# Optimization experiments

Measured on AMD Instinct MI355X. Metric: run time of the kernel, lower is better.

The kernel has to match this reference:

```python
import jax, jax.numpy as jnp
import numpy as np

B, T, D = 1, 2048, 4096
H, G = 32, 8
HD = D // H          # 128
REP = H // G         # 4
KV_DIM = 2 * HD * G  # 2048


def setup_inputs() -> dict:
    key = jax.random.key(0)
    k0, k1, k2, k3 = jax.random.split(key, 4)
    x = jax.random.normal(k0, (B, T, D), dtype=jnp.float32)
    Wq = jax.random.normal(k1, (D, D), dtype=jnp.float32) * 0.02
    Wkv = jax.random.normal(k2, (D, KV_DIM), dtype=jnp.float32) * 0.02
    Wo = jax.random.normal(k3, (D, D), dtype=jnp.float32) * 0.02
    bo = jnp.zeros((D,), dtype=jnp.float32)
    return {"x": x, "Wq": Wq, "Wkv": Wkv, "Wo": Wo, "bo": bo}


def reference(x, Wq, Wkv, Wo, bo):
    b, t, d = x.shape
    # projections (qkv_bias=False)
    q = jnp.dot(x, Wq).reshape(b, t, H, HD).transpose(0, 2, 1, 3)        # (b,H,t,hd)
    kv = jnp.dot(x, Wkv).reshape(b, t, G, 2, HD).transpose(2, 3, 0, 1, 4)  # (G,2,b,t,hd)
    k, v = kv[:, 0], kv[:, 1]                                             # (G,b,t,hd)
    # faithful to torch: unsqueeze+repeat then flat view(b, H, t, hd)
    k = jnp.broadcast_to(k[:, :, None], (G, b, REP, t, HD)).reshape(b, H, t, HD)
    v = jnp.broadcast_to(v[:, :, None], (G, b, REP, t, HD)).reshape(b, H, t, HD)
    # attention: mask then scale, matching original order
    scores = jnp.einsum('bhqd,bhkd->bhqk', q, k)                          # (b,H,t,t)
    causal = jnp.triu(jnp.ones((t, t), dtype=bool), 1)
    scores = jnp.where(causal[None, None], -jnp.inf, scores)
    weights = jax.nn.softmax(scores * (1.0 / HD ** 0.5), axis=-1)
    ctx = jnp.einsum('bhqk,bhkd->bhqd', weights, v)                       # (b,H,t,hd)
    ctx = ctx.transpose(0, 2, 1, 3).reshape(b, t, d)
    return jnp.dot(ctx, Wo) + bo
```

## Files before the change

kernel.cpp:

```cpp
#include <hip/hip_runtime.h>

#define T_SEQ 2048
#define D_MODEL 4096
#define NH 32
#define NG 8
#define HD 128

typedef unsigned short u16;
typedef __bf16 bf16x8 __attribute__((ext_vector_type(8)));
typedef float f32x4 __attribute__((ext_vector_type(4)));

#define AS1 __attribute__((address_space(1)))
#define AS3 __attribute__((address_space(3)))

__device__ __forceinline__ void async_cp16(const u16* g, u16* l) {
  __builtin_amdgcn_global_load_lds((AS1 void*)g, (AS3 void*)l, 16, 0, 0);
}

__device__ __forceinline__ u16 f2bf(float f){
  union { float f; unsigned x; } v; v.f = f;
  unsigned r = v.x + 0x7FFFu + ((v.x >> 16) & 1u);
  return (u16)(r >> 16);
}
__device__ __forceinline__ u16 to_bf(float f){ return f2bf(f); }
__device__ __forceinline__ u16 to_bf(u16 u){ return u; }

__global__ __launch_bounds__(256) void cvt_k(const float* __restrict__ in,
                                             u16* __restrict__ out, int n4)
{
  int i = blockIdx.x * 256 + threadIdx.x;
  if (i >= n4) return;
  float4 v = *(const float4*)&in[(size_t)i * 4];
  short4 o;
  o.x = (short)f2bf(v.x); o.y = (short)f2bf(v.y);
  o.z = (short)f2bf(v.z); o.w = (short)f2bf(v.w);
  *(short4*)&out[(size_t)i * 4] = o;
}

template<typename TIN>
__global__ __launch_bounds__(256) void transpose_k(const TIN* __restrict__ in,
                                                   u16* __restrict__ out, int R, int C)
{
  int z = blockIdx.z;
  in  += (size_t)z * R * C;
  out += (size_t)z * R * C;
  __shared__ __align__(16) u16 tile[32][36];
  int c0 = blockIdx.x * 32, r0 = blockIdx.y * 32;
  int t = threadIdx.x;
  int lr = t >> 3, lc = (t & 7) * 4;
  const TIN* src = &in[(size_t)(r0 + lr) * C + c0 + lc];
  #pragma unroll
  for (int i = 0; i < 4; i++) tile[lr][lc + i] = to_bf(src[i]);
  __syncthreads();
  short4 v;
  v.x = (short)tile[lc + 0][lr];
  v.y = (short)tile[lc + 1][lr];
  v.z = (short)tile[lc + 2][lr];
  v.w = (short)tile[lc + 3][lr];
  *(short4*)&out[(size_t)(c0 + lr) * R + r0 + lc] = v;
}

template<int MODE>
__global__ __launch_bounds__(256) void gemm_k(
    const u16* __restrict__ A, const u16* __restrict__ BT,
    u16* __restrict__ Cout, u16* __restrict__ Kout, u16* __restrict__ Vout,
    float* __restrict__ Fout, const float* __restrict__ bias, int K, int N)
{
  __shared__ __align__(16) u16 sA[2 * 128 * 64];
  __shared__ __align__(16) u16 sB[2 * 128 * 64];
  const int t = threadIdx.x;
  const int lane = t & 63, wave = t >> 6;
  const int quad = lane >> 4, lm = lane & 15;
  const int wm = wave >> 1, wn = wave & 1;
  const int m0 = blockIdx.y * 128, n0 = blockIdx.x * 128;
  const int ntk = K >> 6;
  const f32x4 fzero = {0.f, 0.f, 0.f, 0.f};

  const int sr_sub = lane >> 3;
  const int sgl = (lane & 7) ^ sr_sub;

  f32x4 acc[4][4];
  #pragma unroll
  for (int i = 0; i < 4; i++)
    #pragma unroll
    for (int j = 0; j < 4; j++) acc[i][j] = fzero;

  auto stage = [&](int td) {
    const int k0 = td << 6;
    u16* dA = sA + (td & 1) * (128 * 64);
    u16* dB = sB + (td & 1) * (128 * 64);
    #pragma unroll
    for (int c = 0; c < 4; c++) {
      int r = c * 32 + wave * 8 + sr_sub;
      async_cp16(&A [(size_t)(m0 + r) * K + k0 + sgl * 8], &dA[(c * 256 + wave * 64) * 8]);
      async_cp16(&BT[(size_t)(n0 + r) * K + k0 + sgl * 8], &dB[(c * 256 + wave * 64) * 8]);
    }
  };

  stage(0);
  stage(1);

  for (int ti = 0; ti < ntk; ++ti) {
    if (ti + 1 < ntk) { asm volatile("s_waitcnt vmcnt(8)" ::: "memory"); }
    else             { asm volatile("s_waitcnt vmcnt(0)" ::: "memory"); }
    __builtin_amdgcn_s_barrier();
    asm volatile("" ::: "memory");

    const u16* cA = sA + (ti & 1) * (128 * 64);
    const u16* cB = sB + (ti & 1) * (128 * 64);

    __builtin_amdgcn_s_setprio(1);
    #pragma unroll
    for (int kb = 0; kb < 2; kb++) {
      bf16x8 af[4], bfr[4];
      #pragma unroll
      for (int mt = 0; mt < 4; mt++) {
        int row = wm * 64 + mt * 16 + lm;
        af[mt] = *(const bf16x8*)&cA[row * 64 + (((kb * 4 + quad) ^ (lm & 7)) * 8)];
      }
      #pragma unroll
      for (int nt = 0; nt < 4; nt++) {
        int row = wn * 64 + nt * 16 + lm;
        bfr[nt] = *(const bf16x8*)&cB[row * 64 + (((kb * 4 + quad) ^ (lm & 7)) * 8)];
      }
      #pragma unroll
      for (int mt = 0; mt < 4; mt++)
        #pragma unroll
        for (int nt = 0; nt < 4; nt++)
          acc[mt][nt] = __builtin_amdgcn_mfma_f32_16x16x32_bf16(af[mt], bfr[nt], acc[mt][nt], 0, 0, 0);
    }
    __builtin_amdgcn_s_setprio(0);

    __builtin_amdgcn_s_barrier();
    asm volatile("" ::: "memory");
    if (ti + 2 < ntk) stage(ti + 2);
  }

  #pragma unroll
  for (int mt = 0; mt < 4; mt++) {
    #pragma unroll
    for (int nt = 0; nt < 4; nt++) {
      int gcol = n0 + wn * 64 + nt * 16 + lm;
      int grow0 = m0 + wm * 64 + mt * 16 + quad * 4;
      if (MODE == 1 && ((gcol >> 7) & 1)) {
        int g = gcol >> 8, hd = gcol & 127;
        short4 pv;
        pv.x = (short)f2bf(acc[mt][nt][0]);
        pv.y = (short)f2bf(acc[mt][nt][1]);
        pv.z = (short)f2bf(acc[mt][nt][2]);
        pv.w = (short)f2bf(acc[mt][nt][3]);
        *(short4*)&Vout[((size_t)g * HD + hd) * T_SEQ + grow0] = pv;
      } else {
        #pragma unroll
        for (int r = 0; r < 4; r++) {
          int grow = grow0 + r;
          float v = acc[mt][nt][r];
          if (MODE == 0) {
            Cout[(size_t)grow * N + gcol] = f2bf(v);
          } else if (MODE == 1) {
            int g = gcol >> 8, hd = gcol & 127;
            Kout[((size_t)g * T_SEQ + grow) * HD + hd] = f2bf(v);
          } else {
            Fout[(size_t)grow * N + gcol] = v + bias[gcol];
          }
        }
      }
    }
  }
}

__global__ __launch_bounds__(256) void attn_k(
    const u16* __restrict__ Q, const u16* __restrict__ Kb,
    const u16* __restrict__ Vt, u16* __restrict__ ctx)
{
  __shared__ __align__(16) u16 sK[2 * 64 * 128];
  __shared__ __align__(16) u16 sV[2 * 128 * 64];
  __shared__ __align__(16) u16 sP[4 * 16 * 72];
  const int t = threadIdx.x;
  const int lane = t & 63, wave = t >> 6;
  const int quad = lane >> 4, lm = lane & 15;

  const int id = blockIdx.x + gridDim.x * blockIdx.y;
  const int g = id & 7;
  const int idx = id >> 3;
  const int h = g * 4 + (idx & 3);
  const int q0 = (31 - (idx >> 2)) * 64;
  const int nt = (q0 >> 6) + 1;

  const float scale = 0.088388347648318447f;
  const float C1 = scale * 1.4426950408889634f;
  const float C2 = -14.0f * 1.4426950408889634f;
  const f32x4 fzero = {0.f, 0.f, 0.f, 0.f};

  bf16x8 aq[4];
  {
    const u16* qp = Q + (size_t)(q0 + wave * 16 + lm) * D_MODEL + h * HD + quad * 8;
    #pragma unroll
    for (int kb = 0; kb < 4; kb++) aq[kb] = *(const bf16x8*)(qp + kb * 32);
  }
  f32x4 o[8];
  #pragma unroll
  for (int i = 0; i < 8; i++) o[i] = fzero;
  float l4[4];
  #pragma unroll
  for (int r = 0; r < 4; r++) l4[r] = 0.f;

  const u16* Kg = Kb + (size_t)g * T_SEQ * HD;
  const u16* Vg = Vt + (size_t)g * HD * T_SEQ;
  u16* sPw = sP + wave * 16 * 72;

  const int k_r_sub = lane >> 4;
  const int v_r_sub = lane >> 3;
  const int v_gl = (lane & 7) ^ v_r_sub;

  auto stage = [&](int td) {
    const int kv0 = td << 6;
    u16* dK = sK + (td & 1) * (64 * 128);
    u16* dV = sV + (td & 1) * (128 * 64);
    #pragma unroll
    for (int c = 0; c < 4; c++) {
      int rk = c * 16 + wave * 4 + k_r_sub;
      int kgl = (lane & 15) ^ (rk & 7);
      async_cp16(&Kg[(size_t)(kv0 + rk) * HD + kgl * 8], &dK[(c * 256 + wave * 64) * 8]);
      int rv = c * 32 + wave * 8 + v_r_sub;
      async_cp16(&Vg[(size_t)rv * T_SEQ + kv0 + v_gl * 8], &dV[(c * 256 + wave * 64) * 8]);
    }
  };

  stage(0);
  if (nt > 1) stage(1);

  for (int ti = 0; ti < nt; ++ti) {
    if (ti + 1 < nt) { asm volatile("s_waitcnt vmcnt(8)" ::: "memory"); }
    else             { asm volatile("s_waitcnt vmcnt(0)" ::: "memory"); }
    __builtin_amdgcn_s_barrier();
    asm volatile("" ::: "memory");

    const u16* cK = sK + (ti & 1) * (64 * 128);
    const u16* cV = sV + (ti & 1) * (128 * 64);
    const int kv0 = ti << 6;

    f32x4 s[4];
    __builtin_amdgcn_s_setprio(1);
    #pragma unroll
    for (int nt4 = 0; nt4 < 4; nt4++) {
      s[nt4] = fzero;
      #pragma unroll
      for (int kb = 0; kb < 4; kb++) {
        int row = nt4 * 16 + lm;
        bf16x8 bk = *(const bf16x8*)&cK[row * 128 + (((kb * 4 + quad) ^ (lm & 7)) * 8)];
        s[nt4] = __builtin_amdgcn_mfma_f32_16x16x32_bf16(aq[kb], bk, s[nt4], 0, 0, 0);
      }
    }
    __builtin_amdgcn_s_setprio(0);

    #pragma unroll
    for (int r = 0; r < 4; r++) {
      int qr = q0 + wave * 16 + quad * 4 + r;
      #pragma unroll
      for (int nt4 = 0; nt4 < 4; nt4++) {
        int kvc = kv0 + nt4 * 16 + lm;
        float p = exp2f(fmaf(s[nt4][r], C1, C2));
        p = (kvc > qr) ? 0.f : p;
        l4[r] += p;
        sPw[(quad * 4 + r) * 72 + nt4 * 16 + lm] = f2bf(p);
      }
    }

    __builtin_amdgcn_s_setprio(1);
    #pragma unroll
    for (int kb2 = 0; kb2 < 2; kb2++) {
      bf16x8 ap = *(const bf16x8*)&sPw[lm * 72 + kb2 * 32 + quad * 8];
      #pragma unroll
      for (int n8 = 0; n8 < 8; n8++) {
        int row = n8 * 16 + lm;
        bf16x8 bv = *(const bf16x8*)&cV[row * 64 + (((kb2 * 4 + quad) ^ (lm & 7)) * 8)];
        o[n8] = __builtin_amdgcn_mfma_f32_16x16x32_bf16(ap, bv, o[n8], 0, 0, 0);
      }
    }
    __builtin_amdgcn_s_setprio(0);

    __builtin_amdgcn_s_barrier();
    asm volatile("" ::: "memory");
    if (ti + 2 < nt) stage(ti + 2);
  }

  #pragma unroll
  for (int r = 0; r < 4; r++) {
    #pragma unroll
    for (int off = 1; off < 16; off <<= 1) l4[r] += __shfl_xor(l4[r], off, 64);
  }

  #pragma unroll
  for (int r = 0; r < 4; r++) {
    float inv = 1.f / l4[r];
    #pragma unroll
    for (int n8 = 0; n8 < 8; n8++) {
      ctx[(size_t)(q0 + wave * 16 + quad * 4 + r) * D_MODEL + h * HD + n8 * 16 + lm]
          = f2bf(o[n8][r] * inv);
    }
  }
}

extern "C" void kernel_launch(void* const* d_in, const int* in_sizes, int n_in,
                              void* d_out, int out_size, void* d_ws, size_t ws_size,
                              hipStream_t stream)
{
  const float* x   = (const float*)d_in[0];
  const float* Wq  = (const float*)d_in[1];
  const float* Wkv = (const float*)d_in[2];
  const float* Wo  = (const float*)d_in[3];
  const float* bo  = (const float*)d_in[4];
  float* out = (float*)d_out;

  char* ws = (char*)d_ws;
  const size_t SZ_T   = 33554432;
  const size_t SZ_ACT = 16777216;
  const size_t SZ_KV  = 4194304;
  u16* Tb = (u16*)(ws);
  u16* Xb = (u16*)(ws + SZ_T);
  u16* Qb = (u16*)(ws + SZ_T + SZ_ACT);
  u16* Cx = (u16*)(ws + SZ_T + 2 * SZ_ACT);
  u16* Kb = (u16*)(ws + SZ_T + 3 * SZ_ACT);
  u16* Vt = (u16*)(ws + SZ_T + 3 * SZ_ACT + SZ_KV);

  cvt_k<<<dim3(8192, 1, 1), 256, 0, stream>>>(x, Xb, 2097152);
  transpose_k<float><<<dim3(128, 128, 1), 256, 0, stream>>>(Wq, Tb, 4096, 4096);
  gemm_k<0><<<dim3(32, 16, 1), 256, 0, stream>>>(Xb, Tb, Qb, nullptr, nullptr, nullptr, nullptr, 4096, 4096);
  transpose_k<float><<<dim3(64, 128, 1), 256, 0, stream>>>(Wkv, Tb, 4096, 2048);
  gemm_k<1><<<dim3(16, 16, 1), 256, 0, stream>>>(Xb, Tb, nullptr, Kb, Vt, nullptr, nullptr, 4096, 2048);
  attn_k<<<dim3(32, 32, 1), 256, 0, stream>>>(Qb, Kb, Vt, Cx);
  transpose_k<float><<<dim3(128, 128, 1), 256, 0, stream>>>(Wo, Tb, 4096, 4096);
  gemm_k<2><<<dim3(32, 16, 1), 256, 0, stream>>>(Cx, Tb, nullptr, nullptr, nullptr, out, bo, 4096, 4096);
}
```

Before: 488.8 us.

## Fuse Q and KV projections into one GEMM; compute softmax row sums via MFMA

The Q and KV weight transposes now go into one contiguous buffer, so a single 4096x6144 GEMM launch writes Q, K and transposed V, replacing two separate GEMM launches. In attention, the per-element row-sum accumulation and final shuffle reduction are replaced by an extra MFMA of P against a ones vector. The causal mask comparison now runs only on the diagonal tile. Cx reuses the Xb buffer to keep workspace small. Row sums now come from the bf16-rounded P values rather than the fp32 probabilities, which slightly changes numerics.

```diff
diff --git a/kernel.cpp b/kernel.cpp
--- a/kernel.cpp
+++ b/kernel.cpp
@@ -41,9 +41,6 @@
 __global__ __launch_bounds__(256) void transpose_k(const TIN* __restrict__ in,
                                                    u16* __restrict__ out, int R, int C)
 {
-  int z = blockIdx.z;
-  in  += (size_t)z * R * C;
-  out += (size_t)z * R * C;
   __shared__ __align__(16) u16 tile[32][36];
   int c0 = blockIdx.x * 32, r0 = blockIdx.y * 32;
   int t = threadIdx.x;
@@ -142,28 +139,31 @@
     for (int nt = 0; nt < 4; nt++) {
       int gcol = n0 + wn * 64 + nt * 16 + lm;
       int grow0 = m0 + wm * 64 + mt * 16 + quad * 4;
-      if (MODE == 1 && ((gcol >> 7) & 1)) {
-        int g = gcol >> 8, hd = gcol & 127;
-        short4 pv;
-        pv.x = (short)f2bf(acc[mt][nt][0]);
-        pv.y = (short)f2bf(acc[mt][nt][1]);
-        pv.z = (short)f2bf(acc[mt][nt][2]);
-        pv.w = (short)f2bf(acc[mt][nt][3]);
-        *(short4*)&Vout[((size_t)g * HD + hd) * T_SEQ + grow0] = pv;
+      if (MODE == 1) {
+        if (gcol < 4096) {
+          #pragma unroll
+          for (int r = 0; r < 4; r++)
+            Cout[(size_t)(grow0 + r) * 4096 + gcol] = f2bf(acc[mt][nt][r]);
+        } else {
+          int c = gcol - 4096;
+          int g = c >> 8, s = (c >> 7) & 1, hd = c & 127;
+          if (s) {
+            short4 pv;
+            pv.x = (short)f2bf(acc[mt][nt][0]);
+            pv.y = (short)f2bf(acc[mt][nt][1]);
+            pv.z = (short)f2bf(acc[mt][nt][2]);
+            pv.w = (short)f2bf(acc[mt][nt][3]);
+            *(short4*)&Vout[((size_t)g * HD + hd) * T_SEQ + grow0] = pv;
+          } else {
+            #pragma unroll
+            for (int r = 0; r < 4; r++)
+              Kout[((size_t)g * T_SEQ + grow0 + r) * HD + hd] = f2bf(acc[mt][nt][r]);
+          }
+        }
       } else {
         #pragma unroll
-        for (int r = 0; r < 4; r++) {
-          int grow = grow0 + r;
-          float v = acc[mt][nt][r];
-          if (MODE == 0) {
-            Cout[(size_t)grow * N + gcol] = f2bf(v);
-          } else if (MODE == 1) {
-            int g = gcol >> 8, hd = gcol & 127;
-            Kout[((size_t)g * T_SEQ + grow) * HD + hd] = f2bf(v);
-          } else {
-            Fout[(size_t)grow * N + gcol] = v + bias[gcol];
-          }
-        }
+        for (int r = 0; r < 4; r++)
+          Fout[(size_t)(grow0 + r) * N + gcol] = acc[mt][nt][r] + bias[gcol];
       }
     }
   }
@@ -198,12 +198,14 @@
     #pragma unroll
     for (int kb = 0; kb < 4; kb++) aq[kb] = *(const bf16x8*)(qp + kb * 32);
   }
+  bf16x8 bones;
+  #pragma unroll
+  for (int i = 0; i < 8; i++) bones[i] = (__bf16)1.0f;
+
   f32x4 o[8];
   #pragma unroll
   for (int i = 0; i < 8; i++) o[i] = fzero;
-  float l4[4];
-  #pragma unroll
-  for (int r = 0; r < 4; r++) l4[r] = 0.f;
+  f32x4 lacc = fzero;
 
   const u16* Kg = Kb + (size_t)g * T_SEQ * HD;
   const u16* Vg = Vt + (size_t)g * HD * T_SEQ;
@@ -254,16 +256,26 @@
     }
     __builtin_amdgcn_s_setprio(0);
 
-    #pragma unroll
-    for (int r = 0; r < 4; r++) {
-      int qr = q0 + wave * 16 + quad * 4 + r;
-      #pragma unroll
-      for (int nt4 = 0; nt4 < 4; nt4++) {
-        int kvc = kv0 + nt4 * 16 + lm;
-        float p = exp2f(fmaf(s[nt4][r], C1, C2));
-        p = (kvc > qr) ? 0.f : p;
-        l4[r] += p;
-        sPw[(quad * 4 + r) * 72 + nt4 * 16 + lm] = f2bf(p);
+    if (ti == nt - 1) {
+      #pragma unroll
+      for (int r = 0; r < 4; r++) {
+        int qr = q0 + wave * 16 + quad * 4 + r;
+        #pragma unroll
+        for (int nt4 = 0; nt4 < 4; nt4++) {
+          int kvc = kv0 + nt4 * 16 + lm;
+          float p = exp2f(fmaf(s[nt4][r], C1, C2));
+          p = (kvc > qr) ? 0.f : p;
+          sPw[(quad * 4 + r) * 72 + nt4 * 16 + lm] = f2bf(p);
+        }
+      }
+    } else {
+      #pragma unroll
+      for (int r = 0; r < 4; r++) {
+        #pragma unroll
+        for (int nt4 = 0; nt4 < 4; nt4++) {
+          float p = exp2f(fmaf(s[nt4][r], C1, C2));
+          sPw[(quad * 4 + r) * 72 + nt4 * 16 + lm] = f2bf(p);
+        }
       }
     }
 
@@ -271,6 +283,7 @@
     #pragma unroll
     for (int kb2 = 0; kb2 < 2; kb2++) {
       bf16x8 ap = *(const bf16x8*)&sPw[lm * 72 + kb2 * 32 + quad * 8];
+      lacc = __builtin_amdgcn_mfma_f32_16x16x32_bf16(ap, bones, lacc, 0, 0, 0);
       #pragma unroll
       for (int n8 = 0; n8 < 8; n8++) {
         int row = n8 * 16 + lm;
@@ -287,13 +300,7 @@
 
   #pragma unroll
   for (int r = 0; r < 4; r++) {
-    #pragma unroll
-    for (int off = 1; off < 16; off <<= 1) l4[r] += __shfl_xor(l4[r], off, 64);
-  }
-
-  #pragma unroll
-  for (int r = 0; r < 4; r++) {
-    float inv = 1.f / l4[r];
+    float inv = 1.f / lacc[r];
     #pragma unroll
     for (int n8 = 0; n8 < 8; n8++) {
       ctx[(size_t)(q0 + wave * 16 + quad * 4 + r) * D_MODEL + h * HD + n8 * 16 + lm]
@@ -314,21 +321,20 @@
   float* out = (float*)d_out;
 
   char* ws = (char*)d_ws;
-  const size_t SZ_T   = 33554432;
+  const size_t SZ_T   = 50331648;
   const size_t SZ_ACT = 16777216;
   const size_t SZ_KV  = 4194304;
   u16* Tb = (u16*)(ws);
   u16* Xb = (u16*)(ws + SZ_T);
   u16* Qb = (u16*)(ws + SZ_T + SZ_ACT);
-  u16* Cx = (u16*)(ws + SZ_T + 2 * SZ_ACT);
-  u16* Kb = (u16*)(ws + SZ_T + 3 * SZ_ACT);
-  u16* Vt = (u16*)(ws + SZ_T + 3 * SZ_ACT + SZ_KV);
+  u16* Kb = (u16*)(ws + SZ_T + 2 * SZ_ACT);
+  u16* Vt = (u16*)(ws + SZ_T + 2 * SZ_ACT + SZ_KV);
+  u16* Cx = Xb;
 
   cvt_k<<<dim3(8192, 1, 1), 256, 0, stream>>>(x, Xb, 2097152);
   transpose_k<float><<<dim3(128, 128, 1), 256, 0, stream>>>(Wq, Tb, 4096, 4096);
-  gemm_k<0><<<dim3(32, 16, 1), 256, 0, stream>>>(Xb, Tb, Qb, nullptr, nullptr, nullptr, nullptr, 4096, 4096);
-  transpose_k<float><<<dim3(64, 128, 1), 256, 0, stream>>>(Wkv, Tb, 4096, 2048);
-  gemm_k<1><<<dim3(16, 16, 1), 256, 0, stream>>>(Xb, Tb, nullptr, Kb, Vt, nullptr, nullptr, 4096, 2048);
+  transpose_k<float><<<dim3(64, 128, 1), 256, 0, stream>>>(Wkv, Tb + (size_t)4096 * 4096, 4096, 2048);
+  gemm_k<1><<<dim3(48, 16, 1), 256, 0, stream>>>(Xb, Tb, Qb, Kb, Vt, nullptr, nullptr, 4096, 6144);
   attn_k<<<dim3(32, 32, 1), 256, 0, stream>>>(Qb, Kb, Vt, Cx);
   transpose_k<float><<<dim3(128, 128, 1), 256, 0, stream>>>(Wo, Tb, 4096, 4096);
   gemm_k<2><<<dim3(32, 16, 1), 256, 0, stream>>>(Cx, Tb, nullptr, nullptr, nullptr, out, bo, 4096, 4096);
```

Measured after the change: 473.2 us. 1.03x faster.
